# Kernel optimization log

Hardware: AMD Instinct MI355X
Metric: run time of the kernel (lower is better)

The kernel has to match this reference:

```python
import jax, jax.numpy as jnp
import numpy as np

BETA = 0.2
ALPHA_NEG = 0.8
ALPHA_POS = 0.2
EPS = 1e-8  # torch cosine_similarity eps

B, D, P = 8192, 256, 4096


def setup_inputs() -> dict:
    key = jax.random.key(0)
    k1, k2 = jax.random.split(key)
    embeddings = jax.random.normal(k1, (B, D), dtype=jnp.float32)
    positive_pairs = jax.random.randint(k2, (P, 2), 0, B, dtype=jnp.int32)
    return {"embeddings": embeddings, "positive_pairs": positive_pairs}


def reference(embeddings, positive_pairs):
    b = embeddings.shape[0]
    p = positive_pairs.shape[0]
    # cosine similarity matrix (normalize once, single GEMM)
    nrm = jnp.maximum(jnp.linalg.norm(embeddings, axis=1, keepdims=True), EPS)
    e = embeddings / nrm
    cos = e @ e.T                              # [B, B]
    exp_cos = jnp.exp(cos / BETA)
    ii = positive_pairs[:, 0]
    jj = positive_pairs[:, 1]
    # mask = eye + positive pairs (both directions)
    mask = jnp.eye(b, dtype=bool)
    mask = mask.at[ii, jj].set(True).at[jj, ii].set(True)
    exp_masked = jnp.where(mask, 0.0, exp_cos)  # masked_fill(mask, 0)
    pos_ij = exp_cos[ii, jj]                   # [P]
    pos_ji = exp_cos[jj, ii]                   # [P]
    exp_i = exp_masked[ii]                     # [P, B]
    exp_j = exp_masked[jj]                     # [P, B]
    # hard-negative mining via alpha_neg quantile per row
    thr_i = jnp.quantile(exp_i, ALPHA_NEG, axis=1, keepdims=True)
    thr_j = jnp.quantile(exp_j, ALPHA_NEG, axis=1, keepdims=True)
    S_i = jnp.sum(jnp.where(exp_i >= thr_i, exp_i, 0.0), axis=1)  # [P]
    S_j = jnp.sum(jnp.where(exp_j >= thr_j, exp_j, 0.0), axis=1)  # [P]
    # hard-positive mining via alpha_pos quantile
    thr_pij = jnp.quantile(pos_ij, ALPHA_POS)
    thr_pji = jnp.quantile(pos_ji, ALPHA_POS)
    sel_ij = pos_ij <= thr_pij
    sel_ji = pos_ji <= thr_pji
    # torch loop zips the two (order-preserving) boolean-selected lists ->
    # truncates to min count; values are never cross-coupled, only the count.
    kmin = jnp.minimum(sel_ij.sum(), sel_ji.sum())
    act_ij = sel_ij & ((jnp.cumsum(sel_ij.astype(jnp.int32)) - 1) < kmin)
    act_ji = sel_ji & ((jnp.cumsum(sel_ji.astype(jnp.int32)) - 1) < kmin)
    # -log(pk / (pk + S[m])) = log1p(S[m] / pk), summed over all m per pk
    term_ij = jnp.log1p(S_i[None, :] / pos_ij[:, None])  # [P, P]
    term_ji = jnp.log1p(S_j[None, :] / pos_ji[:, None])  # [P, P]
    loss = (jnp.sum(term_ij * act_ij[:, None].astype(term_ij.dtype))
            + jnp.sum(term_ji * act_ji[:, None].astype(term_ji.dtype)))
    return loss / (2.0 * p)
```

## Files before the change

### kernel.cpp

```cpp
#include <hip/hip_runtime.h>
#include <stdint.h>

#define BN    8192
#define DK    256
#define PN    4096
#define MAXP  16
#define RANK_ASC 6553
#define QSTEP 0.02f

typedef __bf16  bf16_8 __attribute__((ext_vector_type(8)));
typedef __bf16  bf16_4 __attribute__((ext_vector_type(4)));
typedef float   f32x4  __attribute__((ext_vector_type(4)));

__device__ __forceinline__ void gload_lds16(const void* g, void* l) {
  __builtin_amdgcn_global_load_lds(
      (const __attribute__((address_space(1))) unsigned int*)g,
      (__attribute__((address_space(3))) unsigned int*)l, 16, 0, 0);
}

__device__ __forceinline__ void find_bin_256(const unsigned* hist, int rank,
                                             int* sh, unsigned* wtot) {
  const int tid = threadIdx.x, lane = tid & 63, w = tid >> 6;
  unsigned x = hist[tid];
  unsigned pref = x;
  #pragma unroll
  for (int o = 1; o < 64; o <<= 1) {
    unsigned y = __shfl_up(pref, o);
    if (lane >= o) pref += y;
  }
  if (lane == 63) wtot[w] = pref;
  __syncthreads();
  unsigned woff = 0;
  for (int i = 0; i < w; ++i) woff += wtot[i];
  unsigned incl = pref + woff, excl = incl - x;
  if ((unsigned)rank >= excl && (unsigned)rank < incl) { sh[0] = tid; sh[1] = rank - (int)excl; }
  __syncthreads();
}

__device__ __forceinline__ float block_sum4(float x, float* red4) {
  const int lane = threadIdx.x & 63, w = threadIdx.x >> 6;
  #pragma unroll
  for (int o = 32; o; o >>= 1) x += __shfl_xor(x, o);
  __syncthreads();
  if (lane == 0) red4[w] = x;
  __syncthreads();
  return red4[0] + red4[1] + red4[2] + red4[3];
}

__global__ void __launch_bounds__(256) clear_kernel(int* pcount, int* rowlist, int* cnt) {
  const int i = blockIdx.x * 256 + threadIdx.x;
  pcount[i] = 0; rowlist[i] = 0;
  if (i == 0) cnt[0] = 0;
}

__global__ void __launch_bounds__(256) norm_pairs_kernel(
    const float* __restrict__ X, float* __restrict__ E, __bf16* __restrict__ Ebf,
    const int2* __restrict__ pairs, int* pcount, int* partners) {
  const int tid  = threadIdx.x;
  const int lane = tid & 63;
  const int wib  = tid >> 6;
  const int row  = blockIdx.x * 4 + wib;

  float4 x = ((const float4*)(X + (size_t)row * DK))[lane];
  float ss = x.x * x.x + x.y * x.y + x.z * x.z + x.w * x.w;
  #pragma unroll
  for (int o = 32; o; o >>= 1) ss += __shfl_xor(ss, o);
  float nrm = fmaxf(sqrtf(ss), 1e-8f);
  float4 e;
  e.x = x.x / nrm; e.y = x.y / nrm; e.z = x.z / nrm; e.w = x.w / nrm;
  ((float4*)(E + (size_t)row * DK))[lane] = e;
  bf16_4 b;
  b[0] = (__bf16)e.x; b[1] = (__bf16)e.y; b[2] = (__bf16)e.z; b[3] = (__bf16)e.w;
  *(bf16_4*)(Ebf + (size_t)row * DK + lane * 4) = b;

  const int p = blockIdx.x * 256 + tid;
  if (p < PN) {
    int2 pr = pairs[p];
    int ix = atomicAdd(&pcount[pr.x], 1);
    if (ix < MAXP) partners[pr.x * MAXP + ix] = pr.y;
    int iy = atomicAdd(&pcount[pr.y], 1);
    if (iy < MAXP) partners[pr.y * MAXP + iy] = pr.x;
  }
}

__global__ void __launch_bounds__(256) compact_pos_kernel(
    const int* __restrict__ pcount, int* rowlist, int* cnt,
    const float* __restrict__ E, const int2* __restrict__ pairs,
    float* __restrict__ pos) {
  const int tid  = threadIdx.x;
  const int lane = tid & 63;
  const int wib  = tid >> 6;
  const int gix  = blockIdx.x * 256 + tid;

  if (gix < BN && pcount[gix] > 0) {
    int ppos = atomicAdd(cnt, 1);
    rowlist[ppos] = gix;
  }

  const int p = blockIdx.x * 4 + wib;
  int2 pr = pairs[p];
  float4 a = ((const float4*)(E + (size_t)pr.x * DK))[lane];
  float4 b = ((const float4*)(E + (size_t)pr.y * DK))[lane];
  float d = a.x * b.x + a.y * b.y + a.z * b.z + a.w * b.w;
  #pragma unroll
  for (int o = 32; o; o >>= 1) d += __shfl_xor(d, o);
  if (lane == 0) pos[p] = __expf(5.0f * d);
}

__global__ void __launch_bounds__(256) gemm_code_kernel(
    const __bf16* __restrict__ E, const int* __restrict__ rowlist,
    const int* __restrict__ countp, uint32_t* __restrict__ out4) {
  if ((int)blockIdx.y * 128 >= *countp) return;
  __shared__ __align__(16) __bf16 sA[128 * 32];
  __shared__ __align__(16) __bf16 sB[128 * 32];
  const int tid  = threadIdx.x;
  const int lane = tid & 63;
  const int w    = tid >> 6;
  const int wm   = w >> 1, wn = w & 1;
  const int trow = blockIdx.y * 128;
  const int tcol = blockIdx.x * 128;
  const int r0   = tid >> 2;
  const int seg  = tid & 3;

  const int ga0 = rowlist[trow + r0];
  const int ga1 = rowlist[trow + 64 + r0];
  const __bf16* pa0 = E + (size_t)ga0 * DK + seg * 8;
  const __bf16* pa1 = E + (size_t)ga1 * DK + seg * 8;
  const __bf16* pb0 = E + (size_t)(tcol + r0) * DK + seg * 8;
  const __bf16* pb1 = E + (size_t)(tcol + 64 + r0) * DK + seg * 8;
  __bf16* la0 = &sA[tid * 8];
  __bf16* la1 = &sA[2048 + tid * 8];
  __bf16* lb0 = &sB[tid * 8];
  __bf16* lb1 = &sB[2048 + tid * 8];

  f32x4 acc[4][4];
  #pragma unroll
  for (int i = 0; i < 4; ++i)
    #pragma unroll
    for (int j = 0; j < 4; ++j) {
      f32x4 z = {0.f, 0.f, 0.f, 0.f};
      acc[i][j] = z;
    }

  for (int kt = 0; kt < 8; ++kt) {
    const int k0 = kt * 32;
    __syncthreads();
    gload_lds16(pa0 + k0, la0);
    gload_lds16(pa1 + k0, la1);
    gload_lds16(pb0 + k0, lb0);
    gload_lds16(pb1 + k0, lb1);
    __syncthreads();
    bf16_8 af[4], bfg[4];
    #pragma unroll
    for (int q = 0; q < 4; ++q) {
      af[q]  = *(const bf16_8*)&sA[(wm * 64 + q * 16 + (lane & 15)) * 32 + (lane >> 4) * 8];
      bfg[q] = *(const bf16_8*)&sB[(wn * 64 + q * 16 + (lane & 15)) * 32 + (lane >> 4) * 8];
    }
    #pragma unroll
    for (int i = 0; i < 4; ++i)
      #pragma unroll
      for (int j = 0; j < 4; ++j)
        acc[i][j] = __builtin_amdgcn_mfma_f32_16x16x32_bf16(af[i], bfg[j], acc[i][j], 0, 0, 0);
  }

  const int crow = trow + wm * 64 + (lane >> 4) * 4;
  const int ccol = tcol + wn * 64 + (lane & 15);
  #pragma unroll
  for (int i = 0; i < 4; ++i) {
    const int gidx = (crow + i * 16) >> 2;
    #pragma unroll
    for (int j = 0; j < 4; ++j) {
      const int col = ccol + j * 16;
      uint32_t u = 0;
      #pragma unroll
      for (int r = 0; r < 4; ++r) {
        int c = (int)fmaf(acc[i][j][r], 250.0f, 128.5f);
        c = c < 1 ? 1 : (c > 255 ? 255 : c);
        u |= (uint32_t)c << (8 * r);
      }
      out4[(size_t)gidx * BN + col] = u;
    }
  }
}

__global__ void __launch_bounds__(256) row_stats4_kernel(
    const uint32_t* __restrict__ expc4, const int* __restrict__ rowlist,
    const int* __restrict__ countp, const int* __restrict__ pcount,
    const int* __restrict__ partners, float* __restrict__ S) {
  __shared__ unsigned hist[4][4][256];
  __shared__ unsigned total[4][256];
  __shared__ int plist[4][MAXP + 1];
  __shared__ int npl[4];
  __shared__ int growl[4];
  __shared__ int sh[2];
  __shared__ unsigned wtot[4];
  __shared__ float redf[4];
  const int g = blockIdx.x;
  const int cnt = *countp;
  if (g * 4 >= cnt) return;
  const int tid = threadIdx.x, lane = tid & 63, w = tid >> 6;

  uint4 rv[8];
  const uint4* src = (const uint4*)(expc4 + (size_t)g * BN);
  #pragma unroll
  for (int q = 0; q < 8; ++q) rv[q] = src[q * 256 + tid];

  if (tid < 4) {
    int rr = g * 4 + tid;
    int grow = (rr < cnt) ? rowlist[rr] : -1;
    growl[tid] = grow;
    int np = 0;
    if (grow >= 0) {
      np = pcount[grow]; if (np > MAXP) np = MAXP;
      for (int e = 0; e < np; ++e) plist[tid][e] = partners[grow * MAXP + e];
      plist[tid][np] = grow;
      np++;
    }
    npl[tid] = np;
  }
  #pragma unroll
  for (int k = 0; k < 16; ++k) ((unsigned*)hist)[k * 256 + tid] = 0;
  __syncthreads();

  #pragma unroll
  for (int r4 = 0; r4 < 4; ++r4) {
    const int np = npl[r4];
    for (int e = 0; e < np; ++e) {
      int c = plist[r4][e];
      int t = c >> 2;
      if ((t & 255) == tid) {
        unsigned* wp = (unsigned*)&rv[t >> 8];
        wp[c & 3] &= ~(0xFFu << (r4 * 8));
      }
    }
  }

  unsigned* h = (unsigned*)hist[w];
  #pragma unroll
  for (int q = 0; q < 8; ++q) {
    #pragma unroll
    for (int word = 0; word < 4; ++word) {
      unsigned dw = ((const unsigned*)&rv[q])[word];
      atomicAdd(&h[0 * 256 + (dw & 255u)], 1u);
      atomicAdd(&h[1 * 256 + ((dw >> 8) & 255u)], 1u);
      atomicAdd(&h[2 * 256 + ((dw >> 16) & 255u)], 1u);
      atomicAdd(&h[3 * 256 + (dw >> 24)], 1u);
    }
  }
  __syncthreads();
  #pragma unroll
  for (int r4 = 0; r4 < 4; ++r4)
    total[r4][tid] = hist[0][r4][tid] + hist[1][r4][tid] + hist[2][r4][tid] + hist[3][r4][tid];
  __syncthreads();

  const float val = __expf((float)(tid - 128) * QSTEP);
  for (int r4 = 0; r4 < 4; ++r4) {
    find_bin_256(total[r4], RANK_ASC, sh, wtot);
    const int b    = sh[0];
    const int need = (int)total[r4][b] - sh[1];
    float contrib = (tid > b) ? (float)total[r4][tid] * val
                  : (tid == b) ? (float)need * val : 0.f;
    #pragma unroll
    for (int o = 32; o; o >>= 1) contrib += __shfl_xor(contrib, o);
    __syncthreads();
    if (lane == 0) redf[w] = contrib;
    __syncthreads();
    if (tid == 0 && growl[r4] >= 0)
      S[growl[r4]] = redf[0] + redf[1] + redf[2] + redf[3];
    __syncthreads();
  }
}

__global__ void __launch_bounds__(256) finale_kernel(
    const float* __restrict__ pos, const int2* __restrict__ pairs,
    const float* __restrict__ S, float* __restrict__ out) {
  __shared__ uint32_t v[PN];
  __shared__ unsigned hist[256];
  __shared__ int sh[2];
  __shared__ unsigned wtot[4];
  __shared__ float red4[4];
  const int tid = threadIdx.x;
  for (int i = tid; i < PN; i += 256) v[i] = ((const uint32_t*)pos)[i];
  __syncthreads();
  int rank = 819;
  uint32_t prefix = 0;
  for (int pass = 0; pass < 4; ++pass) {
    const int shift = 24 - pass * 8;
    hist[tid] = 0;
    __syncthreads();
    for (int i = tid; i < PN; i += 256) {
      uint32_t x = v[i];
      bool match = (pass == 0) || ((x >> (shift + 8)) == (prefix >> (shift + 8)));
      if (match) atomicAdd(&hist[(x >> shift) & 255u], 1u);
    }
    __syncthreads();
    find_bin_256(hist, rank, sh, wtot);
    prefix |= ((uint32_t)sh[0]) << shift;
    rank = sh[1];
    __syncthreads();
  }
  float thr; __builtin_memcpy(&thr, &prefix, 4);

  float n = 0.f, sl = 0.f, sp = 0.f, sp2 = 0.f;
  for (int r = tid; r < PN; r += 256) {
    float p; uint32_t b = v[r]; __builtin_memcpy(&p, &b, 4);
    if (p <= thr) { n += 1.f; sl += __logf(p); sp += p; sp2 += p * p; }
  }
  float t = 0.f, u = 0.f, vv = 0.f;
  for (int c = tid; c < PN; c += 256) {
    int2 pr = pairs[c];
    float s1 = S[pr.x], s2 = S[pr.y];
    float i1 = 1.f / s1, i2 = 1.f / s2;
    t += __logf(s1) + __logf(s2);
    u += i1 + i2;
    vv += i1 * i1 + i2 * i2;
  }
  const float N   = block_sum4(n, red4);
  const float SL  = block_sum4(sl, red4);
  const float SP  = block_sum4(sp, red4);
  const float SP2 = block_sum4(sp2, red4);
  const float T   = block_sum4(t, red4);
  const float U   = block_sum4(u, red4);
  const float V   = block_sum4(vv, red4);
  if (tid == 0) {
    double num = (double)N * T - 2.0 * (double)PN * (double)SL
               + (double)SP * U - 0.5 * (double)SP2 * V;
    out[0] = (float)(num / (2.0 * (double)PN));
  }
}

extern "C" void kernel_launch(void* const* d_in, const int* in_sizes, int n_in,
                              void* d_out, int out_size, void* d_ws, size_t ws_size,
                              hipStream_t stream) {
  const float* emb  = (const float*)d_in[0];
  const int2* pairs = (const int2*)d_in[1];
  float* out = (float*)d_out;

  char* w = (char*)d_ws;
  size_t off = 0;
  float*    E     = (float*)(w + off);    off += (size_t)BN * DK * 4;
  __bf16*   Ebf   = (__bf16*)(w + off);   off += (size_t)BN * DK * 2;
  float*    S     = (float*)(w + off);    off += (size_t)BN * 4;
  float*    pos   = (float*)(w + off);    off += (size_t)PN * 4;
  int*      pcnt  = (int*)(w + off);      off += (size_t)BN * 4;
  int*      parts = (int*)(w + off);      off += (size_t)BN * MAXP * 4;
  int*      rlist = (int*)(w + off);      off += (size_t)BN * 4;
  int*      cnt   = (int*)(w + off);      off += 256;
  uint32_t* out4  = (uint32_t*)(w + off); off += (size_t)(BN / 4) * BN * 4;

  clear_kernel<<<BN / 256, 256, 0, stream>>>(pcnt, rlist, cnt);
  norm_pairs_kernel<<<BN / 4, 256, 0, stream>>>(emb, E, Ebf, pairs, pcnt, parts);
  compact_pos_kernel<<<PN / 4, 256, 0, stream>>>(pcnt, rlist, cnt, E, pairs, pos);
  gemm_code_kernel<<<dim3(BN / 128, BN / 128), 256, 0, stream>>>(Ebf, rlist, cnt, out4);
  row_stats4_kernel<<<BN / 4, 256, 0, stream>>>(out4, rlist, cnt, pcnt, parts, S);
  finale_kernel<<<1, 256, 0, stream>>>(pos, pairs, S, out);
}
```

Measured before the change: 161.1 us.

## Stage full A tile in LDS once with XOR swizzle, read B directly from global

The GEMM kernel now loads the entire 128x256 A tile (gathered rows) into LDS up front, using an XOR swizzle on 16-byte slots to avoid bank conflicts. B fragments are read straight from global memory instead of being staged through LDS. This removes the per-k-step double __syncthreads and LDS staging for B. In exchange it raises LDS use to 64KB per block, which lowers occupancy, and it puts uncoalesced B loads on the MFMA critical path with no prefetch.

```diff
diff --git a/kernel.cpp b/kernel.cpp
--- a/kernel.cpp
+++ b/kernel.cpp
@@ -111,27 +111,24 @@
     const __bf16* __restrict__ E, const int* __restrict__ rowlist,
     const int* __restrict__ countp, uint32_t* __restrict__ out4) {
   if ((int)blockIdx.y * 128 >= *countp) return;
-  __shared__ __align__(16) __bf16 sA[128 * 32];
-  __shared__ __align__(16) __bf16 sB[128 * 32];
+  __shared__ __align__(16) __bf16 sA[128 * 256];
   const int tid  = threadIdx.x;
   const int lane = tid & 63;
   const int w    = tid >> 6;
   const int wm   = w >> 1, wn = w & 1;
   const int trow = blockIdx.y * 128;
   const int tcol = blockIdx.x * 128;
-  const int r0   = tid >> 2;
-  const int seg  = tid & 3;
-
-  const int ga0 = rowlist[trow + r0];
-  const int ga1 = rowlist[trow + 64 + r0];
-  const __bf16* pa0 = E + (size_t)ga0 * DK + seg * 8;
-  const __bf16* pa1 = E + (size_t)ga1 * DK + seg * 8;
-  const __bf16* pb0 = E + (size_t)(tcol + r0) * DK + seg * 8;
-  const __bf16* pb1 = E + (size_t)(tcol + 64 + r0) * DK + seg * 8;
-  __bf16* la0 = &sA[tid * 8];
-  __bf16* la1 = &sA[2048 + tid * 8];
-  __bf16* lb0 = &sB[tid * 8];
-  __bf16* lb1 = &sB[2048 + tid * 8];
+
+  #pragma unroll
+  for (int i = 0; i < 16; ++i) {
+    const int slin = i * 256 + tid;
+    const int row  = slin >> 5;
+    const int slot = slin & 31;
+    const int sg   = slot ^ (row & 7);
+    const int grow = rowlist[trow + row];
+    gload_lds16(E + (size_t)grow * DK + sg * 8, &sA[(size_t)slin * 8]);
+  }
+  __syncthreads();
 
   f32x4 acc[4][4];
   #pragma unroll
@@ -142,19 +139,18 @@
       acc[i][j] = z;
     }
 
+  const int arow = wm * 64 + (lane & 15);
+  const int bcol = tcol + wn * 64 + (lane & 15);
+  const int ksub = lane >> 4;
+
   for (int kt = 0; kt < 8; ++kt) {
-    const int k0 = kt * 32;
-    __syncthreads();
-    gload_lds16(pa0 + k0, la0);
-    gload_lds16(pa1 + k0, la1);
-    gload_lds16(pb0 + k0, lb0);
-    gload_lds16(pb1 + k0, lb1);
-    __syncthreads();
+    const int sg = kt * 4 + ksub;
     bf16_8 af[4], bfg[4];
     #pragma unroll
     for (int q = 0; q < 4; ++q) {
-      af[q]  = *(const bf16_8*)&sA[(wm * 64 + q * 16 + (lane & 15)) * 32 + (lane >> 4) * 8];
-      bfg[q] = *(const bf16_8*)&sB[(wn * 64 + q * 16 + (lane & 15)) * 32 + (lane >> 4) * 8];
+      const int r = arow + q * 16;
+      af[q] = *(const bf16_8*)&sA[r * 256 + (sg ^ (r & 7)) * 8];
+      bfg[q] = *(const bf16_8*)(E + (size_t)(bcol + q * 16) * DK + sg * 8);
     }
     #pragma unroll
     for (int i = 0; i < 4; ++i)
```

Result: slower. 185.7 us (+15.3%).
